# Kernel optimization log

Hardware: AMD Instinct MI355X
Metric: run time of the kernel (lower is better)

## Reference

```python
import jax, jax.numpy as jnp
import numpy as np


def _local_similar(q, k, kH, kW):
    # q, k: [B, C, H, W] -> scores [B, H, W, kH*kW]
    # Matches similar_forward: zero-padded kH x kW neighborhood dot products.
    B, C, H, W = q.shape
    pH, pW = kH // 2, kW // 2
    kp = jnp.pad(k, ((0, 0), (0, 0), (pH, pH), (pW, pW)))
    scores = [
        jnp.einsum('bchw,bchw->bhw', q, kp[:, :, dh:dh + H, dw:dw + W])
        for dh in range(kH) for dw in range(kW)
    ]
    return jnp.stack(scores, axis=-1)


def _local_weighting(v, w, kH, kW):
    # v: [B, C, H, W], w: [B, H, W, kH*kW] -> out [B, C, H, W]
    # Matches weighting_forward: weighted sum over zero-padded neighborhood.
    B, C, H, W = v.shape
    pH, pW = kH // 2, kW // 2
    vp = jnp.pad(v, ((0, 0), (0, 0), (pH, pH), (pW, pW)))
    out = jnp.zeros_like(v)
    idx = 0
    for dh in range(kH):
        for dw in range(kW):
            out = out + w[..., idx][:, None, :, :] * vp[:, :, dh:dh + H, dw:dw + W]
            idx += 1
    return out


def setup_inputs() -> dict:
    key = jax.random.key(0)
    k1, k2, k3, k4 = jax.random.split(key, 4)
    B, C, H, W = 8, 64, 128, 128
    O = 64  # out_channels
    scale = 1.0 / np.sqrt(C).astype(np.float32)
    x = jax.random.normal(k1, (B, C, H, W), jnp.float32)
    W1 = jax.random.normal(k2, (O, C), jnp.float32) * scale  # conv1 (1x1, no bias)
    W2 = jax.random.normal(k3, (O, C), jnp.float32) * scale  # conv2
    W3 = jax.random.normal(k4, (O, C), jnp.float32) * scale  # conv3
    return {"x": x, "W1": W1, "W2": W2, "W3": W3, "kH": 7, "kW": 7}


def reference(x, W1, W2, W3, kH, kW):
    # 1x1 convs == per-pixel channel matmuls
    q = jnp.einsum('oc,bchw->bohw', W1, x)
    k = jnp.einsum('oc,bchw->bohw', W2, x)
    v = jnp.einsum('oc,bchw->bohw', W3, x)
    scores = _local_similar(q, k, kH, kW)          # [B, H, W, kH*kW]
    w = jax.nn.softmax(scores, axis=-1)
    return _local_weighting(v, w, kH, kW)          # [B, O, H, W]
```

## Files before the change

### kernel.cpp

```cpp
#include <hip/hip_runtime.h>
#include <hip/hip_bf16.h>

#define B_ 8
#define C_ 64
#define H_ 128
#define W_ 128
#define HW_ (H_ * W_)

typedef __attribute__((ext_vector_type(8))) short short8;
typedef __attribute__((ext_vector_type(4))) float float4v;
typedef _Float16 f16x2 __attribute__((ext_vector_type(2)));

static __device__ inline unsigned bfbits(float f) {
    __hip_bfloat16 h = __float2bfloat16(f);
    unsigned short s;
    __builtin_memcpy(&s, &h, 2);
    return (unsigned)s;
}

static __device__ inline float dot2(unsigned a, unsigned b, float c) {
    f16x2 ha, hb;
    __builtin_memcpy(&ha, &a, 4);
    __builtin_memcpy(&hb, &b, 4);
#if __has_builtin(__builtin_amdgcn_fdot2)
    return __builtin_amdgcn_fdot2(ha, hb, c, false);
#else
    return fmaf((float)ha.x, (float)hb.x, fmaf((float)ha.y, (float)hb.y, c));
#endif
}

static __device__ inline float2 up2(unsigned u) {
    f16x2 h;
    __builtin_memcpy(&h, &u, 4);
    return make_float2((float)h.x, (float)h.y);
}

__global__ void repack_w(const float* __restrict__ w1, const float* __restrict__ w2,
                         const float* __restrict__ w3,
                         unsigned short* __restrict__ wBhi, unsigned short* __restrict__ wBlo)
{
    const int i = blockIdx.x * 256 + threadIdx.x;
    if (i >= 12288) return;
    const int j = i & 7, lane = (i >> 3) & 63, ks = (i >> 9) & 1, nt = i >> 10;
    const int o = nt * 16 + (lane & 15);
    const int c = ks * 32 + (lane >> 4) * 8 + j;
    const float* wsel = (o < 64) ? w1 : (o < 128) ? w2 : w3;
    const float w = wsel[(o & 63) * 64 + c];
    const unsigned hb = bfbits(w);
    wBhi[i] = (unsigned short)hb;
    wBlo[i] = (unsigned short)bfbits(w - __uint_as_float(hb << 16));
}

#define XROW_ 68

__global__ __launch_bounds__(512, 4) void proj_qkv(
    const float* __restrict__ x,
    const unsigned short* __restrict__ wBhi, const unsigned short* __restrict__ wBlo,
    _Float16* __restrict__ q, _Float16* __restrict__ k, _Float16* __restrict__ v)
{
    __shared__ float xt[128 * XROW_];
    const int b = blockIdx.y;
    const int px0 = blockIdx.x * 128;
    const int t = threadIdx.x;
    const int lane = t & 63;
    const int wave = t >> 6;
    const int wave_m = wave & 1, wave_n = wave >> 1;
    const int n = lane & 15, kg = lane >> 4;

    const float* xb = x + (size_t)b * C_ * HW_;
    #pragma unroll
    for (int r = 0; r < 4; ++r) {
        const int fi = t + r * 512;
        const int c = fi >> 5;
        const int p4 = (fi & 31) * 4;
        const float4 val = *(const float4*)(xb + (size_t)c * HW_ + px0 + p4);
        xt[(p4 + 0) * XROW_ + c] = val.x;
        xt[(p4 + 1) * XROW_ + c] = val.y;
        xt[(p4 + 2) * XROW_ + c] = val.z;
        xt[(p4 + 3) * XROW_ + c] = val.w;
    }
    __syncthreads();

    float4v acc[3][4];
    #pragma unroll
    for (int tnt = 0; tnt < 3; ++tnt)
        #pragma unroll
        for (int mt = 0; mt < 4; ++mt)
            acc[tnt][mt] = (float4v){0.f, 0.f, 0.f, 0.f};

    const int pxl = wave_m * 64 + n;

    #pragma unroll
    for (int ks = 0; ks < 2; ++ks) {
        short8 ahi[4], alo[4];
        #pragma unroll
        for (int mt = 0; mt < 4; ++mt) {
            const float* xp = xt + (size_t)(pxl + mt * 16) * XROW_ + ks * 32 + kg * 8;
            const float4 xa = *(const float4*)xp;
            const float4 xc = *(const float4*)(xp + 4);
            const float xv[8] = {xa.x, xa.y, xa.z, xa.w, xc.x, xc.y, xc.z, xc.w};
            #pragma unroll
            for (int j = 0; j < 8; ++j) {
                const float f = xv[j];
                const unsigned hb = bfbits(f);
                ahi[mt][j] = (short)hb;
                alo[mt][j] = (short)bfbits(f - __uint_as_float(hb << 16));
            }
        }
        #pragma unroll
        for (int tnt = 0; tnt < 3; ++tnt) {
            const int gnt = wave_n * 3 + tnt;
            const size_t bidx = (((size_t)gnt * 2 + ks) * 64 + lane) * 8;
            short8 bh, bl;
            {
                const uint4 uh = *(const uint4*)(wBhi + bidx);
                const uint4 ul = *(const uint4*)(wBlo + bidx);
                __builtin_memcpy(&bh, &uh, 16);
                __builtin_memcpy(&bl, &ul, 16);
            }
            #pragma unroll
            for (int mt = 0; mt < 4; ++mt) {
                acc[tnt][mt] = __builtin_amdgcn_mfma_f32_16x16x32_bf16(
                    ahi[mt], bh, acc[tnt][mt], 0, 0, 0);
                acc[tnt][mt] = __builtin_amdgcn_mfma_f32_16x16x32_bf16(
                    alo[mt], bh, acc[tnt][mt], 0, 0, 0);
                acc[tnt][mt] = __builtin_amdgcn_mfma_f32_16x16x32_bf16(
                    ahi[mt], bl, acc[tnt][mt], 0, 0, 0);
            }
        }
    }

    #pragma unroll
    for (int tnt = 0; tnt < 3; ++tnt) {
        const int gnt = wave_n * 3 + tnt;
        _Float16* base = (gnt < 4) ? q : (gnt < 8) ? k : v;
        const int chunk = gnt & 3;
        #pragma unroll
        for (int mt = 0; mt < 4; ++mt) {
            const int pxm = px0 + wave_m * 64 + mt * 16 + kg * 4;
            const float4v d = acc[tnt][mt];
            _Float16* p = base + (((size_t)b * 4 + chunk) * HW_ + pxm) * 16 + n;
            #pragma unroll
            for (int r = 0; r < 4; ++r) p[(size_t)r * 16] = (_Float16)d[r];
        }
    }
}

#define HP_ 484
#define PL_ 1948

__global__ __launch_bounds__(512, 4) void local_attn(
    const _Float16* __restrict__ q, const _Float16* __restrict__ k,
    const _Float16* __restrict__ v, float* __restrict__ out)
{
    __shared__ float tile[8 * PL_];
    const int b = blockIdx.z, h0 = blockIdx.y * 16, w0 = blockIdx.x * 16;
    const int t = threadIdx.x;
    const int lane = t & 63, wave = t >> 6;
    const int g = lane & 1;
    const int pixel = wave * 32 + (lane >> 1);
    const int pw = pixel & 15, ph = pixel >> 4;
    const size_t px = (size_t)(h0 + ph) * W_ + (w0 + pw);

    uint4 qv[4];
    #pragma unroll
    for (int pp = 0; pp < 4; ++pp) {
        const int p8 = g * 4 + pp;
        qv[pp] = *(const uint4*)(q + (((size_t)b * 4 + (p8 >> 1)) * HW_ + px) * 16 + (p8 & 1) * 8);
    }

    for (int i = t; i < HP_ * 8; i += 512) {
        const int pix = i >> 3, c8 = i & 7;
        const int r = pix / 22, cl = pix - r * 22;
        const int gh = h0 + r - 3, gw = w0 + cl - 3;
        uint4 val = make_uint4(0u, 0u, 0u, 0u);
        if (gh >= 0 && gh < H_ && gw >= 0 && gw < W_)
            val = *(const uint4*)(k + (((size_t)b * 4 + (c8 >> 1)) * HW_ +
                                       (size_t)gh * W_ + gw) * 16 + (c8 & 1) * 8);
        *(uint4*)(tile + c8 * PL_ + pix * 4) = val;
    }
    __syncthreads();

    uint4 vreg[4];
    #pragma unroll
    for (int r = 0; r < 4; ++r) {
        const int i = t + r * 512;
        const int pix = i >> 3, c8 = i & 7;
        const int rr = pix / 22, cl = pix - rr * 22;
        const int gh = h0 + rr - 3, gw = w0 + cl - 3;
        vreg[r] = make_uint4(0u, 0u, 0u, 0u);
        if (gh >= 0 && gh < H_ && gw >= 0 && gw < W_)
            vreg[r] = *(const uint4*)(v + (((size_t)b * 4 + (c8 >> 1)) * HW_ +
                                           (size_t)gh * W_ + gw) * 16 + (c8 & 1) * 8);
    }

    float sc[49];
    #pragma unroll
    for (int dh = 0; dh < 7; ++dh) {
        #pragma unroll
        for (int dw = 0; dw < 7; ++dw) {
            const int np = ((ph + dh) * 22 + (pw + dw)) * 4;
            float s0 = 0.f, s1 = 0.f, s2 = 0.f, s3 = 0.f;
            #pragma unroll
            for (int pp = 0; pp < 4; ++pp) {
                const uint4 u = *(const uint4*)(tile + (g * 4 + pp) * PL_ + np);
                s0 = dot2(qv[pp].x, u.x, s0);
                s1 = dot2(qv[pp].y, u.y, s1);
                s2 = dot2(qv[pp].z, u.z, s2);
                s3 = dot2(qv[pp].w, u.w, s3);
            }
            sc[dh * 7 + dw] = (s0 + s1) + (s2 + s3);
        }
    }

    #pragma unroll
    for (int i = 0; i < 49; ++i)
        sc[i] += __shfl_xor(sc[i], 1, 64);

    float m = sc[0];
    #pragma unroll
    for (int i = 1; i < 49; ++i) m = fmaxf(m, sc[i]);
    float s = 0.f;
    #pragma unroll
    for (int i = 0; i < 49; ++i) { sc[i] = __expf(sc[i] - m); s += sc[i]; }
    const float inv = 1.f / s;
    #pragma unroll
    for (int i = 0; i < 49; ++i) sc[i] *= inv;

    __syncthreads();

    #pragma unroll
    for (int r = 0; r < 4; ++r) {
        const int i = t + r * 512;
        const int pix = i >> 3, c8 = i & 7;
        *(uint4*)(tile + c8 * PL_ + pix * 4) = vreg[r];
    }
    for (int i = t + 2048; i < HP_ * 8; i += 512) {
        const int pix = i >> 3, c8 = i & 7;
        const int r = pix / 22, cl = pix - r * 22;
        const int gh = h0 + r - 3, gw = w0 + cl - 3;
        uint4 val = make_uint4(0u, 0u, 0u, 0u);
        if (gh >= 0 && gh < H_ && gw >= 0 && gw < W_)
            val = *(const uint4*)(v + (((size_t)b * 4 + (c8 >> 1)) * HW_ +
                                       (size_t)gh * W_ + gw) * 16 + (c8 & 1) * 8);
        *(uint4*)(tile + c8 * PL_ + pix * 4) = val;
    }
    __syncthreads();

    float acc[32];
    #pragma unroll
    for (int c = 0; c < 32; ++c) acc[c] = 0.f;
    #pragma unroll
    for (int dh = 0; dh < 7; ++dh) {
        #pragma unroll
        for (int dw = 0; dw < 7; ++dw) {
            const float wgt = sc[dh * 7 + dw];
            const int np = ((ph + dh) * 22 + (pw + dw)) * 4;
            #pragma unroll
            for (int pp = 0; pp < 4; ++pp) {
                const uint4 u = *(const uint4*)(tile + (g * 4 + pp) * PL_ + np);
                const int a = pp * 8;
                float2 f;
                f = up2(u.x); acc[a + 0] = fmaf(wgt, f.x, acc[a + 0]);
                              acc[a + 1] = fmaf(wgt, f.y, acc[a + 1]);
                f = up2(u.y); acc[a + 2] = fmaf(wgt, f.x, acc[a + 2]);
                              acc[a + 3] = fmaf(wgt, f.y, acc[a + 3]);
                f = up2(u.z); acc[a + 4] = fmaf(wgt, f.x, acc[a + 4]);
                              acc[a + 5] = fmaf(wgt, f.y, acc[a + 5]);
                f = up2(u.w); acc[a + 6] = fmaf(wgt, f.x, acc[a + 6]);
                              acc[a + 7] = fmaf(wgt, f.y, acc[a + 7]);
            }
        }
    }

    #pragma unroll
    for (int pp = 0; pp < 4; ++pp) {
        const int p8 = g * 4 + pp;
        const int ch0 = (p8 >> 1) * 16 + (p8 & 1) * 8;
        #pragma unroll
        for (int j = 0; j < 8; ++j)
            out[((size_t)b * 64 + ch0 + j) * HW_ + px] = acc[pp * 8 + j];
    }
}

extern "C" void kernel_launch(void* const* d_in, const int* in_sizes, int n_in,
                              void* d_out, int out_size, void* d_ws, size_t ws_size,
                              hipStream_t stream) {
    const float* x  = (const float*)d_in[0];
    const float* w1 = (const float*)d_in[1];
    const float* w2 = (const float*)d_in[2];
    const float* w3 = (const float*)d_in[3];

    const size_t NE = (size_t)B_ * 4 * HW_ * 16;
    _Float16* q = (_Float16*)d_ws;
    _Float16* k = q + NE;
    _Float16* v = k + NE;
    unsigned short* wBhi = (unsigned short*)(v + NE);
    unsigned short* wBlo = wBhi + 12288;
    float* o = (float*)d_out;

    repack_w<<<dim3(48), 256, 0, stream>>>(w1, w2, w3, wBhi, wBlo);
    proj_qkv<<<dim3(HW_ / 128, B_), 512, 0, stream>>>(x, wBhi, wBlo, q, k, v);
    local_attn<<<dim3(W_ / 16, H_ / 16, B_), 512, 0, stream>>>(q, k, v, o);
}
```

Before: 142.6 us.

## Use fp16 split-x MFMA with single fp16 weights; prefetch more V tile into registers

The projection switches from a three-term bf16 hi/lo split (three MFMAs per tile) to an fp16 hi/lo split of x against a single fp16 weight (two MFMAs per tile). It also drops the weight low-part buffer and its load. The goal is less MFMA work and less conversion overhead in the QKV projection. Separately, local_attn now prefetches 6 rather than 4 chunks of the V halo tile into registers before the softmax, which raises register pressure. Weight precision drops to fp16 rounding, which risks small accuracy loss.

```diff
diff --git a/kernel.cpp b/kernel.cpp
--- a/kernel.cpp
+++ b/kernel.cpp
@@ -7,16 +7,9 @@
 #define W_ 128
 #define HW_ (H_ * W_)
 
-typedef __attribute__((ext_vector_type(8))) short short8;
+typedef __attribute__((ext_vector_type(8))) _Float16 half8v;
 typedef __attribute__((ext_vector_type(4))) float float4v;
 typedef _Float16 f16x2 __attribute__((ext_vector_type(2)));
-
-static __device__ inline unsigned bfbits(float f) {
-    __hip_bfloat16 h = __float2bfloat16(f);
-    unsigned short s;
-    __builtin_memcpy(&s, &h, 2);
-    return (unsigned)s;
-}
 
 static __device__ inline float dot2(unsigned a, unsigned b, float c) {
     f16x2 ha, hb;
@@ -36,8 +29,7 @@
 }
 
 __global__ void repack_w(const float* __restrict__ w1, const float* __restrict__ w2,
-                         const float* __restrict__ w3,
-                         unsigned short* __restrict__ wBhi, unsigned short* __restrict__ wBlo)
+                         const float* __restrict__ w3, _Float16* __restrict__ wBf)
 {
     const int i = blockIdx.x * 256 + threadIdx.x;
     if (i >= 12288) return;
@@ -45,17 +37,13 @@
     const int o = nt * 16 + (lane & 15);
     const int c = ks * 32 + (lane >> 4) * 8 + j;
     const float* wsel = (o < 64) ? w1 : (o < 128) ? w2 : w3;
-    const float w = wsel[(o & 63) * 64 + c];
-    const unsigned hb = bfbits(w);
-    wBhi[i] = (unsigned short)hb;
-    wBlo[i] = (unsigned short)bfbits(w - __uint_as_float(hb << 16));
+    wBf[i] = (_Float16)wsel[(o & 63) * 64 + c];
 }
 
 #define XROW_ 68
 
 __global__ __launch_bounds__(512, 4) void proj_qkv(
-    const float* __restrict__ x,
-    const unsigned short* __restrict__ wBhi, const unsigned short* __restrict__ wBlo,
+    const float* __restrict__ x, const _Float16* __restrict__ wBf,
     _Float16* __restrict__ q, _Float16* __restrict__ k, _Float16* __restrict__ v)
 {
     __shared__ float xt[128 * XROW_];
@@ -92,7 +80,7 @@
 
     #pragma unroll
     for (int ks = 0; ks < 2; ++ks) {
-        short8 ahi[4], alo[4];
+        half8v ah[4], al[4];
         #pragma unroll
         for (int mt = 0; mt < 4; ++mt) {
             const float* xp = xt + (size_t)(pxl + mt * 16) * XROW_ + ks * 32 + kg * 8;
@@ -102,30 +90,26 @@
             #pragma unroll
             for (int j = 0; j < 8; ++j) {
                 const float f = xv[j];
-                const unsigned hb = bfbits(f);
-                ahi[mt][j] = (short)hb;
-                alo[mt][j] = (short)bfbits(f - __uint_as_float(hb << 16));
+                const _Float16 h = (_Float16)f;
+                ah[mt][j] = h;
+                al[mt][j] = (_Float16)(f - (float)h);
             }
         }
         #pragma unroll
         for (int tnt = 0; tnt < 3; ++tnt) {
             const int gnt = wave_n * 3 + tnt;
             const size_t bidx = (((size_t)gnt * 2 + ks) * 64 + lane) * 8;
-            short8 bh, bl;
+            half8v bfr;
             {
-                const uint4 uh = *(const uint4*)(wBhi + bidx);
-                const uint4 ul = *(const uint4*)(wBlo + bidx);
-                __builtin_memcpy(&bh, &uh, 16);
-                __builtin_memcpy(&bl, &ul, 16);
+                const uint4 u = *(const uint4*)(wBf + bidx);
+                __builtin_memcpy(&bfr, &u, 16);
             }
             #pragma unroll
             for (int mt = 0; mt < 4; ++mt) {
-                acc[tnt][mt] = __builtin_amdgcn_mfma_f32_16x16x32_bf16(
-                    ahi[mt], bh, acc[tnt][mt], 0, 0, 0);
-                acc[tnt][mt] = __builtin_amdgcn_mfma_f32_16x16x32_bf16(
-                    alo[mt], bh, acc[tnt][mt], 0, 0, 0);
-                acc[tnt][mt] = __builtin_amdgcn_mfma_f32_16x16x32_bf16(
-                    ahi[mt], bl, acc[tnt][mt], 0, 0, 0);
+                acc[tnt][mt] = __builtin_amdgcn_mfma_f32_16x16x32_f16(
+                    ah[mt], bfr, acc[tnt][mt], 0, 0, 0);
+                acc[tnt][mt] = __builtin_amdgcn_mfma_f32_16x16x32_f16(
+                    al[mt], bfr, acc[tnt][mt], 0, 0, 0);
             }
         }
     }
@@ -181,9 +165,9 @@
     }
     __syncthreads();
 
-    uint4 vreg[4];
-    #pragma unroll
-    for (int r = 0; r < 4; ++r) {
+    uint4 vreg[6];
+    #pragma unroll
+    for (int r = 0; r < 6; ++r) {
         const int i = t + r * 512;
         const int pix = i >> 3, c8 = i & 7;
         const int rr = pix / 22, cl = pix - rr * 22;
@@ -230,12 +214,12 @@
     __syncthreads();
 
     #pragma unroll
-    for (int r = 0; r < 4; ++r) {
+    for (int r = 0; r < 6; ++r) {
         const int i = t + r * 512;
         const int pix = i >> 3, c8 = i & 7;
         *(uint4*)(tile + c8 * PL_ + pix * 4) = vreg[r];
     }
-    for (int i = t + 2048; i < HP_ * 8; i += 512) {
+    for (int i = t + 3072; i < HP_ * 8; i += 512) {
         const int pix = i >> 3, c8 = i & 7;
         const int r = pix / 22, cl = pix - r * 22;
         const int gh = h0 + r - 3, gw = w0 + cl - 3;
@@ -295,11 +279,10 @@
     _Float16* q = (_Float16*)d_ws;
     _Float16* k = q + NE;
     _Float16* v = k + NE;
-    unsigned short* wBhi = (unsigned short*)(v + NE);
-    unsigned short* wBlo = wBhi + 12288;
+    _Float16* wBf = v + NE;
     float* o = (float*)d_out;
 
-    repack_w<<<dim3(48), 256, 0, stream>>>(w1, w2, w3, wBhi, wBlo);
-    proj_qkv<<<dim3(HW_ / 128, B_), 512, 0, stream>>>(x, wBhi, wBlo, q, k, v);
+    repack_w<<<dim3(48), 256, 0, stream>>>(w1, w2, w3, wBf);
+    proj_qkv<<<dim3(HW_ / 128, B_), 512, 0, stream>>>(x, wBf, q, k, v);
     local_attn<<<dim3(W_ / 16, H_ / 16, B_), 512, 0, stream>>>(q, k, v, o);
 }
```

New measurement: 142.3 us. About the same (-0.2%).
